# Optimization experiments

Measured on AMD Instinct MI355X. Metric: run time of the kernel, lower is better.

Reference implementation:

```python
import math
import jax, jax.numpy as jnp
import numpy as np

N_GAUSS = 1_000_000
EPS = 1e-8


def setup_inputs() -> dict:
    key = jax.random.key(0)
    k1, k2, k3 = jax.random.split(key, 3)
    init_extent = 50.0
    means = (jax.random.uniform(k1, (N_GAUSS, 3), dtype=jnp.float32) - 0.5) * 2.0 * init_extent
    log_scales = jnp.full((N_GAUSS, 3), math.log(0.05), dtype=jnp.float32)
    quats = jax.random.normal(k2, (N_GAUSS, 4), dtype=jnp.float32)
    sh_coeffs = jax.random.normal(k3, (N_GAUSS, 16, 3), dtype=jnp.float32) * 0.01
    opa_logit = math.log(0.1 / 0.9)  # inverse_sigmoid(init_opacity=0.1)
    opacity_camera = jnp.full((N_GAUSS, 1), opa_logit, dtype=jnp.float32)
    opacity_lidar = jnp.full((N_GAUSS, 1), opa_logit, dtype=jnp.float32)
    camera_to_world = jnp.eye(4, dtype=jnp.float32)
    lidar_to_world = jnp.eye(4, dtype=jnp.float32)
    intrinsics = jnp.array([[1000.0, 0.0, 800.0], [0.0, 1000.0, 450.0], [0.0, 0.0, 1.0]], dtype=jnp.float32)
    return dict(means=means, log_scales=log_scales, quats=quats, sh_coeffs=sh_coeffs,
                opacity_camera=opacity_camera, opacity_lidar=opacity_lidar,
                camera_to_world=camera_to_world, intrinsics=intrinsics,
                lidar_to_world=lidar_to_world,
                rgb_width=1600, rgb_height=900, lidar_width=1024, lidar_height=128,
                fov_min_deg=-25, fov_max_deg=3, near_plane=1, far_plane=100)


def _bilinear_scatter(u, v, w, vals, H, W, wrap_u):
    """Scatter vals [N,C] with weights w [N] at continuous pixel coords (u,v)
    using bilinear splatting. Returns [H, W, C+1] (weighted vals, weight sum)."""
    u0 = jnp.floor(u)
    v0 = jnp.floor(v)
    fu = u - u0
    fv = v - v0
    u0i = u0.astype(jnp.int32)
    v0i = v0.astype(jnp.int32)
    acc = jnp.zeros((H * W, vals.shape[-1] + 1), dtype=vals.dtype)
    corners = ((0, 0, (1.0 - fu) * (1.0 - fv)), (1, 0, fu * (1.0 - fv)),
               (0, 1, (1.0 - fu) * fv), (1, 1, fu * fv))
    for du, dv, cw in corners:
        ui = u0i + du
        vi = v0i + dv
        if wrap_u:
            ui = jnp.mod(ui, W)
            ok_u = jnp.ones_like(ui, dtype=bool)
        else:
            ok_u = (ui >= 0) & (ui < W)
        ok = ok_u & (vi >= 0) & (vi < H)
        ww = w * cw * ok.astype(w.dtype)
        idx = jnp.clip(vi, 0, H - 1) * W + jnp.clip(ui, 0, W - 1)
        payload = jnp.concatenate([vals * ww[:, None], ww[:, None]], axis=-1)
        acc = acc.at[idx].add(payload)
    return acc.reshape(H, W, -1)


def reference(means, log_scales, quats, sh_coeffs, opacity_camera, opacity_lidar,
              camera_to_world, intrinsics, lidar_to_world,
              rgb_width, rgb_height, lidar_width, lidar_height,
              fov_min_deg, fov_max_deg, near_plane, far_plane):
    H, W = int(rgb_height), int(rgb_width)
    HL, WL = int(lidar_height), int(lidar_width)
    near = float(near_plane)
    far = float(far_plane)

    # ---- camera (point-splat proxy of gsplat rasterization) ----
    w2c = jnp.linalg.inv(camera_to_world)
    pts_c = means @ w2c[:3, :3].T + w2c[:3, 3]  # [N,3] camera frame
    x, y, z = pts_c[:, 0], pts_c[:, 1], pts_c[:, 2]
    valid_c = (z > near) & (z < far)
    zs = jnp.where(valid_c, z, 1.0)
    u = intrinsics[0, 0] * x / zs + intrinsics[0, 2]
    v = intrinsics[1, 1] * y / zs + intrinsics[1, 2]
    opa_c = jax.nn.sigmoid(jnp.clip(opacity_camera[:, 0], -20.0, 20.0))
    colors = jax.nn.sigmoid(sh_coeffs[:, 0, :])  # DC band, as in render_rgb
    wc = opa_c * valid_c.astype(opa_c.dtype)
    vals_c = jnp.concatenate([colors, z[:, None]], axis=-1)  # [N,4] (rgb, depth)
    acc = _bilinear_scatter(u, v, wc, vals_c, H, W, wrap_u=False)
    wsum = acc[..., 4]
    alpha = jnp.clip(wsum, 0.0, 1.0)
    rgb = acc[..., :3] / (wsum[..., None] + EPS) * alpha[..., None]  # black background
    depth = acc[..., 3] / (wsum + EPS)

    # ---- LiDAR (custom spherical bilinear range-image splat, mean aggregation) ----
    w2l = jnp.linalg.inv(lidar_to_world)
    pts_l = means @ w2l[:3, :3].T + w2l[:3, 3]
    r = jnp.linalg.norm(pts_l, axis=-1)
    az = jnp.arctan2(pts_l[:, 1], pts_l[:, 0])
    el = jnp.arcsin(pts_l[:, 2] / jnp.maximum(r, 1e-6))
    fmin = math.radians(float(fov_min_deg))
    fmax = math.radians(float(fov_max_deg))
    uL = (az / (2.0 * jnp.pi) + 0.5) * WL          # azimuth wraps around
    vL = (fmax - el) / (fmax - fmin) * (HL - 1)    # elevation row
    valid_l = (r > near) & (r < far) & (el >= fmin) & (el <= fmax)
    opa_l = jax.nn.sigmoid(jnp.clip(opacity_lidar[:, 0], -20.0, 20.0))
    wl = opa_l * valid_l.astype(opa_l.dtype)
    acc_l = _bilinear_scatter(uL, vL, wl, r[:, None], HL, WL, wrap_u=True)
    lw = acc_l[..., 1]
    lidar_depth = acc_l[..., 0] / (lw + EPS)  # 'mean' depth aggregation
    lidar_alpha = jnp.clip(lw, 0.0, 1.0)

    return (rgb, depth, alpha, lidar_depth, lidar_alpha)
```

## Files before the change

kernel.cpp:

```cpp
#include <hip/hip_runtime.h>
#include <math.h>

#define EPSV 1e-8f
#define PI_D 3.14159265358979323846

__device__ __forceinline__ void invert4x4_reg(const float* __restrict__ m,
                                              float* __restrict__ out) {
    double a00=m[0], a01=m[1], a02=m[2], a03=m[3];
    double a10=m[4], a11=m[5], a12=m[6], a13=m[7];
    double a20=m[8], a21=m[9], a22=m[10],a23=m[11];
    double a30=m[12],a31=m[13],a32=m[14],a33=m[15];

    double b00 = a00*a11 - a01*a10;
    double b01 = a00*a12 - a02*a10;
    double b02 = a00*a13 - a03*a10;
    double b03 = a01*a12 - a02*a11;
    double b04 = a01*a13 - a03*a11;
    double b05 = a02*a13 - a03*a12;
    double b06 = a20*a31 - a21*a30;
    double b07 = a20*a32 - a22*a30;
    double b08 = a20*a33 - a23*a30;
    double b09 = a21*a32 - a22*a31;
    double b10 = a21*a33 - a23*a31;
    double b11 = a22*a33 - a23*a32;

    double det = b00*b11 - b01*b10 + b02*b09 + b03*b08 - b04*b07 + b05*b06;
    double inv = 1.0 / det;

    out[0]  = (float)(( a11*b11 - a12*b10 + a13*b09) * inv);
    out[1]  = (float)((-a01*b11 + a02*b10 - a03*b09) * inv);
    out[2]  = (float)(( a31*b05 - a32*b04 + a33*b03) * inv);
    out[3]  = (float)((-a21*b05 + a22*b04 - a23*b03) * inv);
    out[4]  = (float)((-a10*b11 + a12*b08 - a13*b07) * inv);
    out[5]  = (float)(( a00*b11 - a02*b08 + a03*b07) * inv);
    out[6]  = (float)((-a30*b05 + a32*b02 - a33*b01) * inv);
    out[7]  = (float)(( a20*b05 - a22*b02 + a23*b01) * inv);
    out[8]  = (float)(( a10*b10 - a11*b08 + a13*b06) * inv);
    out[9]  = (float)((-a00*b10 + a01*b08 - a03*b06) * inv);
    out[10] = (float)(( a30*b04 - a31*b02 + a33*b00) * inv);
    out[11] = (float)((-a20*b04 + a21*b02 - a23*b00) * inv);
    out[12] = (float)((-a10*b09 + a11*b07 - a12*b06) * inv);
    out[13] = (float)(( a00*b09 - a01*b07 + a02*b06) * inv);
    out[14] = (float)((-a30*b03 + a31*b01 - a32*b00) * inv);
    out[15] = (float)(( a20*b03 - a21*b01 + a22*b00) * inv);
}

__global__ void prep_kernel(const float* __restrict__ c2w,
                            const float* __restrict__ l2w,
                            float* __restrict__ ws) {
    if (blockIdx.x == 0 && threadIdx.x == 0) {
        invert4x4_reg(c2w, ws);
        invert4x4_reg(l2w, ws + 16);
    }
}

__device__ __forceinline__ float sigmoid_clipped(float x) {
    #pragma clang fp contract(off)
    x = fminf(fmaxf(x, -20.0f), 20.0f);
    return 1.0f / (1.0f + expf(-x));
}

__global__ __launch_bounds__(256) void scatter_kernel(
    const float* __restrict__ means,
    const float* __restrict__ sh,
    const float* __restrict__ opa_c,
    const float* __restrict__ opa_l,
    const float* __restrict__ intr,
    const float* __restrict__ ws,
    const int* __restrict__ p_W, const int* __restrict__ p_H,
    const int* __restrict__ p_WL, const int* __restrict__ p_HL,
    const int* __restrict__ p_fmin, const int* __restrict__ p_fmax,
    const int* __restrict__ p_near, const int* __restrict__ p_far,
    float* __restrict__ out, int N)
{
    #pragma clang fp contract(off)
    const int T = (N + 1) >> 1;
    const int t = blockIdx.x * blockDim.x + threadIdx.x;
    if (t >= T) return;

    const int W = *p_W, H = *p_H, WL = *p_WL, HL = *p_HL;
    const float nearp = (float)(*p_near);
    const float farp  = (float)(*p_far);
    const double dfmin = (double)(*p_fmin) * PI_D / 180.0;
    const double dfmax = (double)(*p_fmax) * PI_D / 180.0;
    const float ffmin  = (float)dfmin;
    const float ffmax  = (float)dfmax;
    const float denomL = (float)(dfmax - dfmin);
    const float twopi  = (float)(2.0 * PI_D);

    const long long HW = (long long)W * H;
    const long long LHW = (long long)WL * HL;
    const long long depthOff = 3 * HW;
    const long long alphaOff = 4 * HW;
    const long long ldOff    = 5 * HW;
    const long long laOff    = 5 * HW + LHW;

    const float fx = intr[0], cx = intr[2], fy = intr[4], cy = intr[5];
    const float* w2c = ws;
    const float* w2l = ws + 16;

    float mx[2], my[2], mz[2], oc[2], ol[2];
    int   gi[2];
    bool  gv[2];
    #pragma unroll
    for (int k = 0; k < 2; k++) {
        int i = t + k * T;
        gv[k] = (i < N);
        int ii = gv[k] ? i : 0;
        gi[k] = ii;
        mx[k] = means[3 * ii + 0];
        my[k] = means[3 * ii + 1];
        mz[k] = means[3 * ii + 2];
        oc[k] = opa_c[ii];
        ol[k] = opa_l[ii];
    }

    #pragma unroll
    for (int k = 0; k < 2; k++) {
        if (!gv[k]) continue;
        const float px = mx[k], py = my[k], pz = mz[k];

        {
            float x = w2c[0] * px + w2c[1] * py + w2c[2]  * pz + w2c[3];
            float y = w2c[4] * px + w2c[5] * py + w2c[6]  * pz + w2c[7];
            float z = w2c[8] * px + w2c[9] * py + w2c[10] * pz + w2c[11];
            if (z > nearp && z < farp) {
                float u = fx * x / z + cx;
                float v = fy * y / z + cy;
                float wc = sigmoid_clipped(oc[k]);
                const float* shp = sh + 48LL * gi[k];
                float c0 = 1.0f / (1.0f + expf(-shp[0]));
                float c1 = 1.0f / (1.0f + expf(-shp[1]));
                float c2 = 1.0f / (1.0f + expf(-shp[2]));

                float u0f = floorf(u), v0f = floorf(v);
                float fu = u - u0f, fv = v - v0f;
                int u0 = (int)u0f, v0 = (int)v0f;
                #pragma unroll
                for (int c = 0; c < 4; c++) {
                    int du = c & 1, dv = c >> 1;
                    int ui = u0 + du, vi = v0 + dv;
                    if (ui >= 0 && ui < W && vi >= 0 && vi < H) {
                        float cw = (du ? fu : 1.0f - fu) * (dv ? fv : 1.0f - fv);
                        float ww = wc * cw;
                        long long idx = (long long)vi * W + ui;
                        atomicAdd(&out[idx * 3 + 0], c0 * ww);
                        atomicAdd(&out[idx * 3 + 1], c1 * ww);
                        atomicAdd(&out[idx * 3 + 2], c2 * ww);
                        atomicAdd(&out[depthOff + idx], z * ww);
                        atomicAdd(&out[alphaOff + idx], ww);
                    }
                }
            }
        }

        {
            float x = w2l[0] * px + w2l[1] * py + w2l[2]  * pz + w2l[3];
            float y = w2l[4] * px + w2l[5] * py + w2l[6]  * pz + w2l[7];
            float z = w2l[8] * px + w2l[9] * py + w2l[10] * pz + w2l[11];
            float rr = ((x * x) + (y * y)) + (z * z);
            float r = sqrtf(rr);
            float q  = z / fmaxf(r, 1e-6f);
            float el = (float)asin((double)q);
            if (r > nearp && r < farp && el >= ffmin && el <= ffmax) {
                float az = (float)atan2((double)y, (double)x);
                float uL = (az / twopi + 0.5f) * (float)WL;
                float vL = (ffmax - el) / denomL * (float)(HL - 1);
                float wl = sigmoid_clipped(ol[k]);

                float u0f = floorf(uL), v0f = floorf(vL);
                float fu = uL - u0f, fv = vL - v0f;
                int u0 = (int)u0f, v0 = (int)v0f;
                #pragma unroll
                for (int c = 0; c < 4; c++) {
                    int du = c & 1, dv = c >> 1;
                    int ui = u0 + du, vi = v0 + dv;
                    if (ui >= WL) ui -= WL;
                    if (vi >= 0 && vi < HL) {
                        float cw = (du ? fu : 1.0f - fu) * (dv ? fv : 1.0f - fv);
                        float ww = wl * cw;
                        long long idx = (long long)vi * WL + ui;
                        atomicAdd(&out[ldOff + idx], r * ww);
                        atomicAdd(&out[laOff + idx], ww);
                    }
                }
            }
        }
    }
}

__global__ __launch_bounds__(256) void finalize_kernel(
    float* __restrict__ out,
    const int* __restrict__ p_W, const int* __restrict__ p_H,
    const int* __restrict__ p_WL, const int* __restrict__ p_HL)
{
    const int W = *p_W, H = *p_H, WL = *p_WL, HL = *p_HL;
    const long long HW = (long long)W * H;
    const long long LHW = (long long)WL * HL;
    const long long depthOff = 3 * HW;
    const long long alphaOff = 4 * HW;
    const long long ldOff    = 5 * HW;
    const long long laOff    = 5 * HW + LHW;

    long long i = (long long)blockIdx.x * blockDim.x + threadIdx.x;
    if (i < HW) {
        float wsum = out[alphaOff + i];
        float a = fminf(fmaxf(wsum, 0.0f), 1.0f);
        float inv = 1.0f / (wsum + EPSV);
        float s = inv * a;
        out[3 * i + 0] *= s;
        out[3 * i + 1] *= s;
        out[3 * i + 2] *= s;
        out[depthOff + i] *= inv;
        out[alphaOff + i] = a;
    }
    if (i < LHW) {
        float wsum = out[laOff + i];
        out[ldOff + i] *= 1.0f / (wsum + EPSV);
        out[laOff + i] = fminf(fmaxf(wsum, 0.0f), 1.0f);
    }
}

extern "C" void kernel_launch(void* const* d_in, const int* in_sizes, int n_in,
                              void* d_out, int out_size, void* d_ws, size_t ws_size,
                              hipStream_t stream) {
    const float* means  = (const float*)d_in[0];
    const float* sh     = (const float*)d_in[3];
    const float* opa_c  = (const float*)d_in[4];
    const float* opa_l  = (const float*)d_in[5];
    const float* c2w    = (const float*)d_in[6];
    const float* intr   = (const float*)d_in[7];
    const float* l2w    = (const float*)d_in[8];
    const int* p_W    = (const int*)d_in[9];
    const int* p_H    = (const int*)d_in[10];
    const int* p_WL   = (const int*)d_in[11];
    const int* p_HL   = (const int*)d_in[12];
    const int* p_fmin = (const int*)d_in[13];
    const int* p_fmax = (const int*)d_in[14];
    const int* p_near = (const int*)d_in[15];
    const int* p_far  = (const int*)d_in[16];

    const int N = in_sizes[0] / 3;
    float* out = (float*)d_out;
    float* ws  = (float*)d_ws;

    hipMemsetAsync(d_out, 0, (size_t)out_size * sizeof(float), stream);

    prep_kernel<<<1, 64, 0, stream>>>(c2w, l2w, ws);

    const int T = (N + 1) / 2;
    scatter_kernel<<<(T + 255) / 256, 256, 0, stream>>>(
        means, sh, opa_c, opa_l, intr, ws,
        p_W, p_H, p_WL, p_HL, p_fmin, p_fmax, p_near, p_far,
        out, N);

    const long long HW = 1600LL * 900LL;
    finalize_kernel<<<(int)((HW + 255) / 256), 256, 0, stream>>>(
        out, p_W, p_H, p_WL, p_HL);
}
```

Baseline: 423.6 us.

## Interleave per-pixel accumulators in workspace buffer for atomic locality

Moves the scatter accumulation from the planar output buffer into a workspace buffer with interleaved per-pixel records (8 floats per camera pixel, 2 per LiDAR pixel). All five atomics for a pixel then land in one cache line instead of three separate planes, and the finalize pass reads them back with vector loads. The inverted matrices move to a device global so the workspace can be used entirely for accumulators. Fallbacks cover smaller workspaces, at the cost of a larger memset and extra code paths.

```diff
diff --git a/kernel.cpp b/kernel.cpp
--- a/kernel.cpp
+++ b/kernel.cpp
@@ -3,6 +3,8 @@
 
 #define EPSV 1e-8f
 #define PI_D 3.14159265358979323846
+
+__device__ float g_mats[32];
 
 __device__ __forceinline__ void invert4x4_reg(const float* __restrict__ m,
                                               float* __restrict__ out) {
@@ -46,11 +48,10 @@
 }
 
 __global__ void prep_kernel(const float* __restrict__ c2w,
-                            const float* __restrict__ l2w,
-                            float* __restrict__ ws) {
+                            const float* __restrict__ l2w) {
     if (blockIdx.x == 0 && threadIdx.x == 0) {
-        invert4x4_reg(c2w, ws);
-        invert4x4_reg(l2w, ws + 16);
+        invert4x4_reg(c2w, g_mats);
+        invert4x4_reg(l2w, g_mats + 16);
     }
 }
 
@@ -60,18 +61,19 @@
     return 1.0f / (1.0f + expf(-x));
 }
 
-__global__ __launch_bounds__(256) void scatter_kernel(
+template<int MODE>
+__global__ __launch_bounds__(256) void scatter_acc(
     const float* __restrict__ means,
     const float* __restrict__ sh,
     const float* __restrict__ opa_c,
     const float* __restrict__ opa_l,
     const float* __restrict__ intr,
-    const float* __restrict__ ws,
+    float* __restrict__ acc,
     const int* __restrict__ p_W, const int* __restrict__ p_H,
     const int* __restrict__ p_WL, const int* __restrict__ p_HL,
     const int* __restrict__ p_fmin, const int* __restrict__ p_fmax,
     const int* __restrict__ p_near, const int* __restrict__ p_far,
-    float* __restrict__ out, int N)
+    int N)
 {
     #pragma clang fp contract(off)
     const int T = (N + 1) >> 1;
@@ -89,15 +91,14 @@
     const float twopi  = (float)(2.0 * PI_D);
 
     const long long HW = (long long)W * H;
-    const long long LHW = (long long)WL * HL;
-    const long long depthOff = 3 * HW;
-    const long long alphaOff = 4 * HW;
-    const long long ldOff    = 5 * HW;
-    const long long laOff    = 5 * HW + LHW;
+
+    float* C  = acc;
+    float* Wp = (MODE == 4) ? (C + 4 * HW) : nullptr;
+    float* L  = C + (MODE == 8 ? 8 : 5) * HW;
 
     const float fx = intr[0], cx = intr[2], fy = intr[4], cy = intr[5];
-    const float* w2c = ws;
-    const float* w2l = ws + 16;
+    const float* w2c = g_mats;
+    const float* w2l = g_mats + 16;
 
     float mx[2], my[2], mz[2], oc[2], ol[2];
     int   gi[2];
@@ -120,6 +121,175 @@
         if (!gv[k]) continue;
         const float px = mx[k], py = my[k], pz = mz[k];
 
+        {
+            float x = w2c[0] * px + w2c[1] * py + w2c[2]  * pz + w2c[3];
+            float y = w2c[4] * px + w2c[5] * py + w2c[6]  * pz + w2c[7];
+            float z = w2c[8] * px + w2c[9] * py + w2c[10] * pz + w2c[11];
+            if (z > nearp && z < farp) {
+                float u = fx * x / z + cx;
+                float v = fy * y / z + cy;
+                float wc = sigmoid_clipped(oc[k]);
+                const float* shp = sh + 48LL * gi[k];
+                float c0 = 1.0f / (1.0f + expf(-shp[0]));
+                float c1 = 1.0f / (1.0f + expf(-shp[1]));
+                float c2 = 1.0f / (1.0f + expf(-shp[2]));
+
+                float u0f = floorf(u), v0f = floorf(v);
+                float fu = u - u0f, fv = v - v0f;
+                int u0 = (int)u0f, v0 = (int)v0f;
+                #pragma unroll
+                for (int c = 0; c < 4; c++) {
+                    int du = c & 1, dv = c >> 1;
+                    int ui = u0 + du, vi = v0 + dv;
+                    if (ui >= 0 && ui < W && vi >= 0 && vi < H) {
+                        float cw = (du ? fu : 1.0f - fu) * (dv ? fv : 1.0f - fv);
+                        float ww = wc * cw;
+                        long long idx = (long long)vi * W + ui;
+                        float* g = C + idx * (MODE == 8 ? 8 : 4);
+                        atomicAdd(g + 0, c0 * ww);
+                        atomicAdd(g + 1, c1 * ww);
+                        atomicAdd(g + 2, c2 * ww);
+                        atomicAdd(g + 3, z * ww);
+                        if (MODE == 8) atomicAdd(g + 4, ww);
+                        else           atomicAdd(Wp + idx, ww);
+                    }
+                }
+            }
+        }
+
+        {
+            float x = w2l[0] * px + w2l[1] * py + w2l[2]  * pz + w2l[3];
+            float y = w2l[4] * px + w2l[5] * py + w2l[6]  * pz + w2l[7];
+            float z = w2l[8] * px + w2l[9] * py + w2l[10] * pz + w2l[11];
+            float rr = ((x * x) + (y * y)) + (z * z);
+            float r = sqrtf(rr);
+            float q  = z / fmaxf(r, 1e-6f);
+            float el = (float)asin((double)q);
+            if (r > nearp && r < farp && el >= ffmin && el <= ffmax) {
+                float az = (float)atan2((double)y, (double)x);
+                float uL = (az / twopi + 0.5f) * (float)WL;
+                float vL = (ffmax - el) / denomL * (float)(HL - 1);
+                float wl = sigmoid_clipped(ol[k]);
+
+                float u0f = floorf(uL), v0f = floorf(vL);
+                float fu = uL - u0f, fv = vL - v0f;
+                int u0 = (int)u0f, v0 = (int)v0f;
+                #pragma unroll
+                for (int c = 0; c < 4; c++) {
+                    int du = c & 1, dv = c >> 1;
+                    int ui = u0 + du, vi = v0 + dv;
+                    if (ui >= WL) ui -= WL;
+                    if (vi >= 0 && vi < HL) {
+                        float cw = (du ? fu : 1.0f - fu) * (dv ? fv : 1.0f - fv);
+                        float ww = wl * cw;
+                        long long idx = (long long)vi * WL + ui;
+                        atomicAdd(L + 2 * idx + 0, r * ww);
+                        atomicAdd(L + 2 * idx + 1, ww);
+                    }
+                }
+            }
+        }
+    }
+}
+
+template<int MODE>
+__global__ __launch_bounds__(256) void finalize_acc(
+    const float* __restrict__ acc,
+    float* __restrict__ out,
+    const int* __restrict__ p_W, const int* __restrict__ p_H,
+    const int* __restrict__ p_WL, const int* __restrict__ p_HL)
+{
+    const int W = *p_W, H = *p_H, WL = *p_WL, HL = *p_HL;
+    const long long HW = (long long)W * H;
+    const long long LHW = (long long)WL * HL;
+    const long long depthOff = 3 * HW;
+    const long long alphaOff = 4 * HW;
+    const long long ldOff    = 5 * HW;
+    const long long laOff    = 5 * HW + LHW;
+
+    const float* C  = acc;
+    const float* Wp = (MODE == 4) ? (C + 4 * HW) : nullptr;
+    const float* L  = C + (MODE == 8 ? 8 : 5) * HW;
+
+    long long i = (long long)blockIdx.x * blockDim.x + threadIdx.x;
+    if (i < HW) {
+        const float* g = C + i * (MODE == 8 ? 8 : 4);
+        float4 p = *reinterpret_cast<const float4*>(g);
+        float wsum = (MODE == 8) ? g[4] : Wp[i];
+        float a = fminf(fmaxf(wsum, 0.0f), 1.0f);
+        float inv = 1.0f / (wsum + EPSV);
+        float s = inv * a;
+        out[3 * i + 0] = p.x * s;
+        out[3 * i + 1] = p.y * s;
+        out[3 * i + 2] = p.z * s;
+        out[depthOff + i] = p.w * inv;
+        out[alphaOff + i] = a;
+    }
+    if (i < LHW) {
+        float2 l = *reinterpret_cast<const float2*>(L + 2 * i);
+        out[ldOff + i] = l.x * (1.0f / (l.y + EPSV));
+        out[laOff + i] = fminf(fmaxf(l.y, 0.0f), 1.0f);
+    }
+}
+
+__global__ __launch_bounds__(256) void scatter_fb(
+    const float* __restrict__ means,
+    const float* __restrict__ sh,
+    const float* __restrict__ opa_c,
+    const float* __restrict__ opa_l,
+    const float* __restrict__ intr,
+    const int* __restrict__ p_W, const int* __restrict__ p_H,
+    const int* __restrict__ p_WL, const int* __restrict__ p_HL,
+    const int* __restrict__ p_fmin, const int* __restrict__ p_fmax,
+    const int* __restrict__ p_near, const int* __restrict__ p_far,
+    float* __restrict__ out, int N)
+{
+    #pragma clang fp contract(off)
+    const int T = (N + 1) >> 1;
+    const int t = blockIdx.x * blockDim.x + threadIdx.x;
+    if (t >= T) return;
+
+    const int W = *p_W, H = *p_H, WL = *p_WL, HL = *p_HL;
+    const float nearp = (float)(*p_near);
+    const float farp  = (float)(*p_far);
+    const double dfmin = (double)(*p_fmin) * PI_D / 180.0;
+    const double dfmax = (double)(*p_fmax) * PI_D / 180.0;
+    const float ffmin  = (float)dfmin;
+    const float ffmax  = (float)dfmax;
+    const float denomL = (float)(dfmax - dfmin);
+    const float twopi  = (float)(2.0 * PI_D);
+
+    const long long HW = (long long)W * H;
+    const long long LHW = (long long)WL * HL;
+    const long long depthOff = 3 * HW;
+    const long long alphaOff = 4 * HW;
+    const long long ldOff    = 5 * HW;
+    const long long laOff    = 5 * HW + LHW;
+
+    const float fx = intr[0], cx = intr[2], fy = intr[4], cy = intr[5];
+    const float* w2c = g_mats;
+    const float* w2l = g_mats + 16;
+
+    float mx[2], my[2], mz[2], oc[2], ol[2];
+    int   gi[2];
+    bool  gv[2];
+    #pragma unroll
+    for (int k = 0; k < 2; k++) {
+        int i = t + k * T;
+        gv[k] = (i < N);
+        int ii = gv[k] ? i : 0;
+        gi[k] = ii;
+        mx[k] = means[3 * ii + 0];
+        my[k] = means[3 * ii + 1];
+        mz[k] = means[3 * ii + 2];
+        oc[k] = opa_c[ii];
+        ol[k] = opa_l[ii];
+    }
+
+    #pragma unroll
+    for (int k = 0; k < 2; k++) {
+        if (!gv[k]) continue;
+        const float px = mx[k], py = my[k], pz = mz[k];
         {
             float x = w2c[0] * px + w2c[1] * py + w2c[2]  * pz + w2c[3];
             float y = w2c[4] * px + w2c[5] * py + w2c[6]  * pz + w2c[7];
@@ -153,7 +323,6 @@
                 }
             }
         }
-
         {
             float x = w2l[0] * px + w2l[1] * py + w2l[2]  * pz + w2l[3];
             float y = w2l[4] * px + w2l[5] * py + w2l[6]  * pz + w2l[7];
@@ -189,7 +358,7 @@
     }
 }
 
-__global__ __launch_bounds__(256) void finalize_kernel(
+__global__ __launch_bounds__(256) void finalize_fb(
     float* __restrict__ out,
     const int* __restrict__ p_W, const int* __restrict__ p_H,
     const int* __restrict__ p_WL, const int* __restrict__ p_HL)
@@ -242,19 +411,40 @@
 
     const int N = in_sizes[0] / 3;
     float* out = (float*)d_out;
-    float* ws  = (float*)d_ws;
-
-    hipMemsetAsync(d_out, 0, (size_t)out_size * sizeof(float), stream);
-
-    prep_kernel<<<1, 64, 0, stream>>>(c2w, l2w, ws);
+    float* acc = (float*)d_ws;
+
+    const long long HW  = 1600LL * 900LL;
+    const long long LHW = 1024LL * 128LL;
+    const size_t bytes8 = (8 * (size_t)HW + 2 * (size_t)LHW) * sizeof(float);
+    const size_t bytes4 = (5 * (size_t)HW + 2 * (size_t)LHW) * sizeof(float);
 
     const int T = (N + 1) / 2;
-    scatter_kernel<<<(T + 255) / 256, 256, 0, stream>>>(
-        means, sh, opa_c, opa_l, intr, ws,
-        p_W, p_H, p_WL, p_HL, p_fmin, p_fmax, p_near, p_far,
-        out, N);
-
-    const long long HW = 1600LL * 900LL;
-    finalize_kernel<<<(int)((HW + 255) / 256), 256, 0, stream>>>(
-        out, p_W, p_H, p_WL, p_HL);
-}
+    const int sgrid = (T + 255) / 256;
+    const int fgrid = (int)((HW + 255) / 256);
+
+    prep_kernel<<<1, 64, 0, stream>>>(c2w, l2w);
+
+    if (ws_size >= bytes8) {
+        hipMemsetAsync(d_ws, 0, bytes8, stream);
+        scatter_acc<8><<<sgrid, 256, 0, stream>>>(
+            means, sh, opa_c, opa_l, intr, acc,
+            p_W, p_H, p_WL, p_HL, p_fmin, p_fmax, p_near, p_far, N);
+        finalize_acc<8><<<fgrid, 256, 0, stream>>>(
+            acc, out, p_W, p_H, p_WL, p_HL);
+    } else if (ws_size >= bytes4) {
+        hipMemsetAsync(d_ws, 0, bytes4, stream);
+        scatter_acc<4><<<sgrid, 256, 0, stream>>>(
+            means, sh, opa_c, opa_l, intr, acc,
+            p_W, p_H, p_WL, p_HL, p_fmin, p_fmax, p_near, p_far, N);
+        finalize_acc<4><<<fgrid, 256, 0, stream>>>(
+            acc, out, p_W, p_H, p_WL, p_HL);
+    } else {
+        hipMemsetAsync(d_out, 0, (size_t)out_size * sizeof(float), stream);
+        scatter_fb<<<sgrid, 256, 0, stream>>>(
+            means, sh, opa_c, opa_l, intr,
+            p_W, p_H, p_WL, p_HL, p_fmin, p_fmax, p_near, p_far,
+            out, N);
+        finalize_fb<<<fgrid, 256, 0, stream>>>(
+            out, p_W, p_H, p_WL, p_HL);
+    }
+}
```

After: 434.2 us. +2.5%, slower.
